# Performance work log

Hardware: AMD Instinct MI355X
Metric: run time of the kernel (lower is better)

Reference implementation:

```python
import jax, jax.numpy as jnp
import numpy as np

N_NODES = 100000
N_EDGES = 1600000
D_IN = 64
D_OUT = 64
EDGE_DIM = 1


def setup_inputs() -> dict:
    key = jax.random.key(0)
    ks = jax.random.split(key, 6)
    x = jax.random.normal(ks[0], (N_NODES, D_IN), dtype=jnp.float32)
    edge_index = jax.random.randint(ks[1], (2, N_EDGES), 0, N_NODES, dtype=jnp.int64)
    edge_attr = jax.random.uniform(ks[2], (N_EDGES, EDGE_DIM), dtype=jnp.float32)
    # xavier-uniform-ish weight
    limit = float(np.sqrt(6.0 / (D_IN + D_OUT)))
    weight = jax.random.uniform(ks[3], (D_IN, D_OUT), minval=-limit, maxval=limit, dtype=jnp.float32)
    lim2 = float(np.sqrt(1.0 / EDGE_DIM))
    ew_W = jax.random.uniform(ks[4], (EDGE_DIM, D_OUT), minval=-lim2, maxval=lim2, dtype=jnp.float32)
    ew_b = jnp.zeros((D_OUT,), dtype=jnp.float32)
    bias = jnp.zeros((D_OUT,), dtype=jnp.float32)
    return {"x": x, "edge_index": edge_index, "edge_attr": edge_attr,
            "weight": weight, "ew_W": ew_W, "ew_b": ew_b, "bias": bias}


def reference(x, edge_index, edge_attr, weight, ew_W, ew_b, bias):
    n_nodes = x.shape[0]
    src = edge_index[0]  # i: message source
    dst = edge_index[1]  # j: message destination
    x_t = x @ weight                                   # [N, D_OUT]
    edge_w = jax.nn.sigmoid(edge_attr @ ew_W + ew_b)   # [E, D_OUT]
    msg = x_t[src] * edge_w                            # [E, D_OUT] gather-multiply
    out = jax.ops.segment_sum(msg, dst, num_segments=n_nodes)  # scatter-add
    return out + bias
```

## Files before the change

kernel.cpp:

```cpp
#include <hip/hip_runtime.h>
#include <hip/hip_bf16.h>
#include <math.h>

#define D 64
#define SCAN_B 256

typedef __hip_bfloat16 bf16;
typedef __attribute__((ext_vector_type(8))) short bf16x8;
typedef __attribute__((ext_vector_type(4))) float f32x4;
typedef __attribute__((ext_vector_type(2))) float f32x2;

static __device__ __forceinline__ short f2bf(float f) {
    unsigned u = __float_as_uint(f);
    u = (u + 0x7FFFu + ((u >> 16) & 1u)) >> 16;
    return (short)u;
}
static __device__ __forceinline__ float bf2f(unsigned short h) {
    return __uint_as_float(((unsigned)h) << 16);
}
static __device__ __forceinline__ float fsig(float a, float nwd, float nbd) {
    float e = __expf(fmaf(a, nwd, nbd));
    return __builtin_amdgcn_rcpf(1.f + e);
}

__global__ __launch_bounds__(256) void gemm_hist_kernel(const float* __restrict__ x,
                                                        const float* __restrict__ W,
                                                        const int* __restrict__ ei,
                                                        bf16* __restrict__ xt,
                                                        int* __restrict__ counts,
                                                        int* __restrict__ rank,
                                                        int n_nodes, int n_edges) {
    __shared__ float Ws[64 * 64];
    {
        const float4* src = reinterpret_cast<const float4*>(W);
        float4* dstp = reinterpret_cast<float4*>(Ws);
        for (int i = threadIdx.x; i < 1024; i += 256) dstp[i] = src[i];
    }

    const int gid = blockIdx.x * blockDim.x + threadIdx.x;
    const int nth = gridDim.x * blockDim.x;

    for (int e = gid; e < n_edges; e += nth) {
        int dst = ei[n_edges + e];
        rank[e] = atomicAdd(&counts[dst], 1);
    }

    __syncthreads();

    const int lane  = threadIdx.x & 63;
    const int wv    = threadIdx.x >> 6;
    const int m0    = blockIdx.x * 64 + wv * 16;
    const int half  = lane >> 4;
    const int idx16 = lane & 15;
    const int k0    = half * 8;

    bf16x8 bfrag[4][2];
#pragma unroll
    for (int t = 0; t < 4; ++t) {
#pragma unroll
        for (int h = 0; h < 2; ++h) {
            bf16x8 f;
#pragma unroll
            for (int j = 0; j < 8; ++j)
                f[j] = f2bf(Ws[(h * 32 + k0 + j) * 64 + t * 16 + idx16]);
            bfrag[t][h] = f;
        }
    }

    const int am = m0 + idx16;
    const bool valid = (am < n_nodes);
    const float* arow = x + (size_t)(valid ? am : 0) * 64;

    f32x4 acc[4] = {{0.f, 0.f, 0.f, 0.f}, {0.f, 0.f, 0.f, 0.f},
                    {0.f, 0.f, 0.f, 0.f}, {0.f, 0.f, 0.f, 0.f}};

#pragma unroll
    for (int h = 0; h < 2; ++h) {
        bf16x8 afrag = {0, 0, 0, 0, 0, 0, 0, 0};
        if (valid) {
            float4 p0 = *reinterpret_cast<const float4*>(arow + h * 32 + k0);
            float4 p1 = *reinterpret_cast<const float4*>(arow + h * 32 + k0 + 4);
            afrag[0] = f2bf(p0.x); afrag[1] = f2bf(p0.y);
            afrag[2] = f2bf(p0.z); afrag[3] = f2bf(p0.w);
            afrag[4] = f2bf(p1.x); afrag[5] = f2bf(p1.y);
            afrag[6] = f2bf(p1.z); afrag[7] = f2bf(p1.w);
        }
#pragma unroll
        for (int t = 0; t < 4; ++t)
            acc[t] = __builtin_amdgcn_mfma_f32_16x16x32_bf16(afrag, bfrag[t][h],
                                                             acc[t], 0, 0, 0);
    }

    const int srow0 = m0 + half * 4;
#pragma unroll
    for (int r = 0; r < 4; ++r) {
        int row = srow0 + r;
        if (row < n_nodes) {
#pragma unroll
            for (int t = 0; t < 4; ++t)
                xt[(size_t)row * 64 + t * 16 + idx16] = __float2bfloat16(acc[t][r]);
        }
    }
}

__global__ __launch_bounds__(SCAN_B) void scan1_kernel(const int* __restrict__ c,
                                                       int* __restrict__ excl,
                                                       int* __restrict__ partials,
                                                       int n) {
    __shared__ int s[SCAN_B];
    int i = blockIdx.x * SCAN_B + threadIdx.x;
    int v = (i < n) ? c[i] : 0;
    s[threadIdx.x] = v;
    __syncthreads();
    for (int off = 1; off < SCAN_B; off <<= 1) {
        int t = (threadIdx.x >= off) ? s[threadIdx.x - off] : 0;
        __syncthreads();
        s[threadIdx.x] += t;
        __syncthreads();
    }
    if (i < n) excl[i] = s[threadIdx.x] - v;
    if (threadIdx.x == SCAN_B - 1) partials[blockIdx.x] = s[SCAN_B - 1];
}

__global__ __launch_bounds__(SCAN_B) void scan23_kernel(int* __restrict__ offsets,
                                                        const int* __restrict__ partials,
                                                        int n, int n_edges) {
    __shared__ int red[SCAN_B];
    int psum = 0;
    for (int i = threadIdx.x; i < blockIdx.x; i += SCAN_B) psum += partials[i];
    red[threadIdx.x] = psum;
    __syncthreads();
    for (int off = SCAN_B / 2; off > 0; off >>= 1) {
        if (threadIdx.x < off) red[threadIdx.x] += red[threadIdx.x + off];
        __syncthreads();
    }
    int base = red[0];
    int i = blockIdx.x * SCAN_B + threadIdx.x;
    if (i < n) offsets[i] += base;
    if (blockIdx.x == 0 && threadIdx.x == 0) offsets[n] = n_edges;
}

__global__ __launch_bounds__(256) void fill_kernel(const int* __restrict__ ei,
                                                   const float* __restrict__ ea,
                                                   const int* __restrict__ offs,
                                                   const int* __restrict__ rank,
                                                   int2* __restrict__ csr,
                                                   int n_edges) {
    int e = blockIdx.x * blockDim.x + threadIdx.x;
    if (e >= n_edges) return;
    int dst = ei[n_edges + e];
    int pos = offs[dst] + rank[e];
    long long v = ((long long)__float_as_int(ea[e]) << 32) | (unsigned)ei[e];
    __builtin_nontemporal_store(v, (long long*)(csr + pos));
}

__global__ __launch_bounds__(256) void gather_kernel(const int* __restrict__ offsets,
                                                     const int2* __restrict__ csr,
                                                     const bf16* __restrict__ xt,
                                                     const float* __restrict__ ewW,
                                                     const float* __restrict__ ewb,
                                                     const float* __restrict__ bias,
                                                     float* __restrict__ out,
                                                     int n_nodes) {
    const int lane  = threadIdx.x & 63;
    const int halfw = lane >> 5;
    const int l     = lane & 31;
    const int d0    = l * 2;
    const int wavei = (blockIdx.x * blockDim.x + threadIdx.x) >> 6;
    const int node  = wavei * 2 + halfw;
    if (node >= n_nodes) return;

    const float2 wv = *reinterpret_cast<const float2*>(ewW + d0);
    const float2 bv = *reinterpret_cast<const float2*>(ewb + d0);
    const float nw0 = -wv.x, nb0 = -bv.x;
    const float nw1 = -wv.y, nb1 = -bv.y;

    const int start = offsets[node];
    const int end   = offsets[node + 1];

    float acc0 = 0.f, acc1 = 0.f;
    int k = start;
    for (; k + 8 <= end; k += 8) {
        long long q[8];
        ushort2 rv[8];
#pragma unroll
        for (int j = 0; j < 8; ++j)
            q[j] = __builtin_nontemporal_load((const long long*)(csr + k + j));
#pragma unroll
        for (int j = 0; j < 8; ++j) {
            unsigned off = (((unsigned)(int)(unsigned)q[j]) << 6) + d0;
            rv[j] = *reinterpret_cast<const ushort2*>(xt + off);
        }
#pragma unroll
        for (int j = 0; j < 8; ++j) {
            float a = __int_as_float((int)(q[j] >> 32));
            acc0 = fmaf(bf2f(rv[j].x), fsig(a, nw0, nb0), acc0);
            acc1 = fmaf(bf2f(rv[j].y), fsig(a, nw1, nb1), acc1);
        }
    }
    for (; k + 4 <= end; k += 4) {
        long long q[4];
        ushort2 rv[4];
#pragma unroll
        for (int j = 0; j < 4; ++j)
            q[j] = __builtin_nontemporal_load((const long long*)(csr + k + j));
#pragma unroll
        for (int j = 0; j < 4; ++j) {
            unsigned off = (((unsigned)(int)(unsigned)q[j]) << 6) + d0;
            rv[j] = *reinterpret_cast<const ushort2*>(xt + off);
        }
#pragma unroll
        for (int j = 0; j < 4; ++j) {
            float a = __int_as_float((int)(q[j] >> 32));
            acc0 = fmaf(bf2f(rv[j].x), fsig(a, nw0, nb0), acc0);
            acc1 = fmaf(bf2f(rv[j].y), fsig(a, nw1, nb1), acc1);
        }
    }
    for (; k < end; ++k) {
        long long q = __builtin_nontemporal_load((const long long*)(csr + k));
        unsigned off = (((unsigned)(int)(unsigned)q) << 6) + d0;
        ushort2 rv = *reinterpret_cast<const ushort2*>(xt + off);
        float a = __int_as_float((int)(q >> 32));
        acc0 = fmaf(bf2f(rv.x), fsig(a, nw0, nb0), acc0);
        acc1 = fmaf(bf2f(rv.y), fsig(a, nw1, nb1), acc1);
    }
    f32x2 o;
    o.x = acc0 + bias[d0];
    o.y = acc1 + bias[d0 + 1];
    __builtin_nontemporal_store(o, reinterpret_cast<f32x2*>(out + (size_t)node * 64 + d0));
}

__global__ __launch_bounds__(256) void init_out_kernel(float* __restrict__ out,
                                                       const float* __restrict__ bias,
                                                       int n_f4) {
    int i = blockIdx.x * blockDim.x + threadIdx.x;
    if (i >= n_f4) return;
    float4 b4 = reinterpret_cast<const float4*>(bias)[i & 15];
    reinterpret_cast<float4*>(out)[i] = b4;
}

__global__ __launch_bounds__(256) void edge_atomic_kernel(const int* __restrict__ ei,
                                                          const float* __restrict__ ea,
                                                          const bf16* __restrict__ xt,
                                                          const float* __restrict__ ewW,
                                                          const float* __restrict__ ewb,
                                                          float* __restrict__ out,
                                                          int n_edges) {
    const int gid = blockIdx.x * blockDim.x + threadIdx.x;
    const int d0 = (gid & 15) * 4;
    int e = gid >> 4;
    const int estride = (gridDim.x * blockDim.x) >> 4;
    for (; e < n_edges; e += estride) {
        const int src = ei[e];
        const int dst = ei[n_edges + e];
        const float a = ea[e];
        float xv0 = __bfloat162float(xt[(size_t)src * 64 + d0 + 0]);
        float xv1 = __bfloat162float(xt[(size_t)src * 64 + d0 + 1]);
        float xv2 = __bfloat162float(xt[(size_t)src * 64 + d0 + 2]);
        float xv3 = __bfloat162float(xt[(size_t)src * 64 + d0 + 3]);
        float w0 = fsig(a, -ewW[d0 + 0], -ewb[d0 + 0]);
        float w1 = fsig(a, -ewW[d0 + 1], -ewb[d0 + 1]);
        float w2 = fsig(a, -ewW[d0 + 2], -ewb[d0 + 2]);
        float w3 = fsig(a, -ewW[d0 + 3], -ewb[d0 + 3]);
        float* op = out + (size_t)dst * 64 + d0;
        unsafeAtomicAdd(op + 0, xv0 * w0);
        unsafeAtomicAdd(op + 1, xv1 * w1);
        unsafeAtomicAdd(op + 2, xv2 * w2);
        unsafeAtomicAdd(op + 3, xv3 * w3);
    }
}

extern "C" void kernel_launch(void* const* d_in, const int* in_sizes, int n_in,
                              void* d_out, int out_size, void* d_ws, size_t ws_size,
                              hipStream_t stream) {
    const float* x      = (const float*)d_in[0];
    const int*   ei     = (const int*)d_in[1];
    const float* ea     = (const float*)d_in[2];
    const float* weight = (const float*)d_in[3];
    const float* ewW    = (const float*)d_in[4];
    const float* ewb    = (const float*)d_in[5];
    const float* bias   = (const float*)d_in[6];
    float* out = (float*)d_out;

    const int n_nodes = in_sizes[0] / D;
    const int n_edges = in_sizes[2];

    char* ws = (char*)d_ws;
    const size_t xt_bytes   = (size_t)n_nodes * D * sizeof(bf16);
    const size_t off_off    = (xt_bytes + 7) & ~(size_t)7;
    const size_t off_bytes  = ((size_t)n_nodes + 4) * sizeof(int);
    const size_t part_off   = off_off + off_bytes;
    const size_t part_bytes = 512 * sizeof(int);
    const size_t rank_off   = part_off + part_bytes;
    const size_t rank_bytes = (size_t)n_edges * sizeof(int);
    size_t csr_off          = (rank_off + rank_bytes + 7) & ~(size_t)7;
    const size_t csr_bytes  = (size_t)n_edges * sizeof(int2);
    const size_t need       = csr_off + csr_bytes;

    bf16* xt   = (bf16*)(ws);
    int*  offs = (int*)(ws + off_off);
    int*  parts= (int*)(ws + part_off);
    int*  rank = (int*)(ws + rank_off);
    int2* csr  = (int2*)(ws + csr_off);

    const bool have_ws = (ws_size >= need);
    const int gemm_grid = (n_nodes + 63) / 64;

    if (have_ws) {
        (void)hipMemsetAsync(offs, 0, off_bytes, stream);
        gemm_hist_kernel<<<gemm_grid, 256, 0, stream>>>(x, weight, ei, xt, offs, rank,
                                                        n_nodes, n_edges);

        const int nscan_blocks = (n_nodes + SCAN_B - 1) / SCAN_B;
        scan1_kernel<<<nscan_blocks, SCAN_B, 0, stream>>>(offs, offs, parts, n_nodes);
        scan23_kernel<<<nscan_blocks, SCAN_B, 0, stream>>>(offs, parts, n_nodes, n_edges);
        fill_kernel<<<(n_edges + 255) / 256, 256, 0, stream>>>(ei, ea, offs, rank, csr, n_edges);

        const int n_waves = (n_nodes + 1) / 2;
        const int gth = n_waves * 64;
        gather_kernel<<<(gth + 255) / 256, 256, 0, stream>>>(offs, csr, xt, ewW, ewb,
                                                             bias, out, n_nodes);
    } else {
        gemm_hist_kernel<<<gemm_grid, 256, 0, stream>>>(x, weight, ei, xt,
                                                        nullptr, nullptr, n_nodes, 0);
        int n_f4 = n_nodes * (D / 4);
        init_out_kernel<<<(n_f4 + 255) / 256, 256, 0, stream>>>(out, bias, n_f4);
        edge_atomic_kernel<<<4096, 256, 0, stream>>>(ei, ea, xt, ewW, ewb, out, n_edges);
    }
}
```

Measured before the change: 189.8 us.

## Split histogram into dedicated blocks and widen gather to four nodes per wave

The fused GEMM+histogram kernel now gives the edge-count atomics to 512 dedicated blocks, and the remaining blocks do only the GEMM, so the two jobs no longer run back to back inside every block. The gather kernel now handles four nodes per wave with 16 lanes each, so each lane loads four bf16 features per gathered row. This halves the number of gather waves and widens each row load, at the cost of more registers per lane and sigmoid work serialised per lane. With fewer lanes per node, load imbalance from uneven node degrees may rise.

```diff
diff --git a/kernel.cpp b/kernel.cpp
--- a/kernel.cpp
+++ b/kernel.cpp
@@ -8,7 +8,6 @@
 typedef __hip_bfloat16 bf16;
 typedef __attribute__((ext_vector_type(8))) short bf16x8;
 typedef __attribute__((ext_vector_type(4))) float f32x4;
-typedef __attribute__((ext_vector_type(2))) float f32x2;
 
 static __device__ __forceinline__ short f2bf(float f) {
     unsigned u = __float_as_uint(f);
@@ -29,27 +28,31 @@
                                                         bf16* __restrict__ xt,
                                                         int* __restrict__ counts,
                                                         int* __restrict__ rank,
-                                                        int n_nodes, int n_edges) {
+                                                        int n_nodes, int n_edges,
+                                                        int hist_blocks) {
     __shared__ float Ws[64 * 64];
+
+    if ((int)blockIdx.x < hist_blocks) {
+        const int gid = blockIdx.x * blockDim.x + threadIdx.x;
+        const int nth = hist_blocks * blockDim.x;
+        for (int e = gid; e < n_edges; e += nth) {
+            int dst = ei[n_edges + e];
+            rank[e] = atomicAdd(&counts[dst], 1);
+        }
+        return;
+    }
+
+    const int bid = blockIdx.x - hist_blocks;
     {
         const float4* src = reinterpret_cast<const float4*>(W);
         float4* dstp = reinterpret_cast<float4*>(Ws);
         for (int i = threadIdx.x; i < 1024; i += 256) dstp[i] = src[i];
     }
-
-    const int gid = blockIdx.x * blockDim.x + threadIdx.x;
-    const int nth = gridDim.x * blockDim.x;
-
-    for (int e = gid; e < n_edges; e += nth) {
-        int dst = ei[n_edges + e];
-        rank[e] = atomicAdd(&counts[dst], 1);
-    }
-
     __syncthreads();
 
     const int lane  = threadIdx.x & 63;
     const int wv    = threadIdx.x >> 6;
-    const int m0    = blockIdx.x * 64 + wv * 16;
+    const int m0    = bid * 64 + wv * 16;
     const int half  = lane >> 4;
     const int idx16 = lane & 15;
     const int k0    = half * 8;
@@ -163,71 +166,79 @@
                                                      float* __restrict__ out,
                                                      int n_nodes) {
     const int lane  = threadIdx.x & 63;
-    const int halfw = lane >> 5;
-    const int l     = lane & 31;
-    const int d0    = l * 2;
+    const int sub   = lane >> 4;
+    const int l     = lane & 15;
+    const int d0    = l * 4;
     const int wavei = (blockIdx.x * blockDim.x + threadIdx.x) >> 6;
-    const int node  = wavei * 2 + halfw;
+    const int node  = wavei * 4 + sub;
     if (node >= n_nodes) return;
 
-    const float2 wv = *reinterpret_cast<const float2*>(ewW + d0);
-    const float2 bv = *reinterpret_cast<const float2*>(ewb + d0);
-    const float nw0 = -wv.x, nb0 = -bv.x;
-    const float nw1 = -wv.y, nb1 = -bv.y;
+    const float4 wv4 = *reinterpret_cast<const float4*>(ewW + d0);
+    const float4 bv4 = *reinterpret_cast<const float4*>(ewb + d0);
+    const float nw0 = -wv4.x, nw1 = -wv4.y, nw2 = -wv4.z, nw3 = -wv4.w;
+    const float nb0 = -bv4.x, nb1 = -bv4.y, nb2 = -bv4.z, nb3 = -bv4.w;
 
     const int start = offsets[node];
     const int end   = offsets[node + 1];
 
-    float acc0 = 0.f, acc1 = 0.f;
+    float acc0 = 0.f, acc1 = 0.f, acc2 = 0.f, acc3 = 0.f;
     int k = start;
     for (; k + 8 <= end; k += 8) {
         long long q[8];
-        ushort2 rv[8];
+        ushort4 rv[8];
 #pragma unroll
         for (int j = 0; j < 8; ++j)
             q[j] = __builtin_nontemporal_load((const long long*)(csr + k + j));
 #pragma unroll
         for (int j = 0; j < 8; ++j) {
             unsigned off = (((unsigned)(int)(unsigned)q[j]) << 6) + d0;
-            rv[j] = *reinterpret_cast<const ushort2*>(xt + off);
+            rv[j] = *reinterpret_cast<const ushort4*>(xt + off);
         }
 #pragma unroll
         for (int j = 0; j < 8; ++j) {
             float a = __int_as_float((int)(q[j] >> 32));
             acc0 = fmaf(bf2f(rv[j].x), fsig(a, nw0, nb0), acc0);
             acc1 = fmaf(bf2f(rv[j].y), fsig(a, nw1, nb1), acc1);
+            acc2 = fmaf(bf2f(rv[j].z), fsig(a, nw2, nb2), acc2);
+            acc3 = fmaf(bf2f(rv[j].w), fsig(a, nw3, nb3), acc3);
         }
     }
     for (; k + 4 <= end; k += 4) {
         long long q[4];
-        ushort2 rv[4];
+        ushort4 rv[4];
 #pragma unroll
         for (int j = 0; j < 4; ++j)
             q[j] = __builtin_nontemporal_load((const long long*)(csr + k + j));
 #pragma unroll
         for (int j = 0; j < 4; ++j) {
             unsigned off = (((unsigned)(int)(unsigned)q[j]) << 6) + d0;
-            rv[j] = *reinterpret_cast<const ushort2*>(xt + off);
+            rv[j] = *reinterpret_cast<const ushort4*>(xt + off);
         }
 #pragma unroll
         for (int j = 0; j < 4; ++j) {
             float a = __int_as_float((int)(q[j] >> 32));
             acc0 = fmaf(bf2f(rv[j].x), fsig(a, nw0, nb0), acc0);
             acc1 = fmaf(bf2f(rv[j].y), fsig(a, nw1, nb1), acc1);
+            acc2 = fmaf(bf2f(rv[j].z), fsig(a, nw2, nb2), acc2);
+            acc3 = fmaf(bf2f(rv[j].w), fsig(a, nw3, nb3), acc3);
         }
     }
     for (; k < end; ++k) {
         long long q = __builtin_nontemporal_load((const long long*)(csr + k));
         unsigned off = (((unsigned)(int)(unsigned)q) << 6) + d0;
-        ushort2 rv = *reinterpret_cast<const ushort2*>(xt + off);
+        ushort4 rv = *reinterpret_cast<const ushort4*>(xt + off);
         float a = __int_as_float((int)(q >> 32));
         acc0 = fmaf(bf2f(rv.x), fsig(a, nw0, nb0), acc0);
         acc1 = fmaf(bf2f(rv.y), fsig(a, nw1, nb1), acc1);
-    }
-    f32x2 o;
-    o.x = acc0 + bias[d0];
+        acc2 = fmaf(bf2f(rv.z), fsig(a, nw2, nb2), acc2);
+        acc3 = fmaf(bf2f(rv.w), fsig(a, nw3, nb3), acc3);
+    }
+    f32x4 o;
+    o.x = acc0 + bias[d0 + 0];
     o.y = acc1 + bias[d0 + 1];
-    __builtin_nontemporal_store(o, reinterpret_cast<f32x2*>(out + (size_t)node * 64 + d0));
+    o.z = acc2 + bias[d0 + 2];
+    o.w = acc3 + bias[d0 + 3];
+    __builtin_nontemporal_store(o, reinterpret_cast<f32x4*>(out + (size_t)node * 64 + d0));
 }
 
 __global__ __launch_bounds__(256) void init_out_kernel(float* __restrict__ out,
@@ -304,25 +315,27 @@
     int2* csr  = (int2*)(ws + csr_off);
 
     const bool have_ws = (ws_size >= need);
-    const int gemm_grid = (n_nodes + 63) / 64;
+    const int gemm_blocks = (n_nodes + 63) / 64;
+    const int hist_blocks = 512;
 
     if (have_ws) {
         (void)hipMemsetAsync(offs, 0, off_bytes, stream);
-        gemm_hist_kernel<<<gemm_grid, 256, 0, stream>>>(x, weight, ei, xt, offs, rank,
-                                                        n_nodes, n_edges);
+        gemm_hist_kernel<<<hist_blocks + gemm_blocks, 256, 0, stream>>>(
+            x, weight, ei, xt, offs, rank, n_nodes, n_edges, hist_blocks);
 
         const int nscan_blocks = (n_nodes + SCAN_B - 1) / SCAN_B;
         scan1_kernel<<<nscan_blocks, SCAN_B, 0, stream>>>(offs, offs, parts, n_nodes);
         scan23_kernel<<<nscan_blocks, SCAN_B, 0, stream>>>(offs, parts, n_nodes, n_edges);
         fill_kernel<<<(n_edges + 255) / 256, 256, 0, stream>>>(ei, ea, offs, rank, csr, n_edges);
 
-        const int n_waves = (n_nodes + 1) / 2;
+        const int n_waves = (n_nodes + 3) / 4;
         const int gth = n_waves * 64;
         gather_kernel<<<(gth + 255) / 256, 256, 0, stream>>>(offs, csr, xt, ewW, ewb,
                                                              bias, out, n_nodes);
     } else {
-        gemm_hist_kernel<<<gemm_grid, 256, 0, stream>>>(x, weight, ei, xt,
-                                                        nullptr, nullptr, n_nodes, 0);
+        gemm_hist_kernel<<<gemm_blocks, 256, 0, stream>>>(x, weight, ei, xt,
+                                                          nullptr, nullptr,
+                                                          n_nodes, 0, 0);
         int n_f4 = n_nodes * (D / 4);
         init_out_kernel<<<(n_f4 + 255) / 256, 256, 0, stream>>>(out, bias, n_f4);
         edge_atomic_kernel<<<4096, 256, 0, stream>>>(ei, ea, xt, ewW, ewb, out, n_edges);
```

New measurement: 187.4 us. No clear change (-1.2%).
